# Kernel tuning notes

Measured on AMD Instinct MI355X. Metric: run time of the kernel, lower is better.

Reference implementation:

```python
import jax, jax.numpy as jnp
import numpy as np

DT = 0.1

def setup_inputs() -> dict:
    key = jax.random.key(0)
    ks = jax.random.split(key, 11)
    B, I, H = 65536, 128, 256
    return {
        "x": jax.random.normal(ks[0], (B, I), jnp.float32),
        "prev_input": jax.random.normal(ks[1], (B, I), jnp.float32),
        "hidden": jax.random.normal(ks[2], (B, H), jnp.float32),
        "W_in_w": jax.random.normal(ks[3], (H, I), jnp.float32) * 0.05,
        "W_in_b": jax.random.normal(ks[4], (H,), jnp.float32) * 0.05,
        "W_rec_w": jax.random.normal(ks[5], (H, H), jnp.float32) * 0.05,
        "W_rec_b": jax.random.normal(ks[6], (H,), jnp.float32) * 0.05,
        "attn_w": jax.random.normal(ks[7], (H, H), jnp.float32) * 0.05,
        "attn_b": jax.random.normal(ks[8], (H,), jnp.float32) * 0.05,
        "ev_w": jax.random.normal(ks[9], (1, 2 * I), jnp.float32) * 0.05,
        "ev_b": jax.random.normal(ks[10], (1,), jnp.float32) * 0.05,
        "tau": jnp.ones((H,), jnp.float32),
    }

def reference(x, prev_input, hidden, W_in_w, W_in_b, W_rec_w, W_rec_b,
              attn_w, attn_b, ev_w, ev_b, tau):
    # event detection from concatenated current + previous input
    event_input = jnp.concatenate([x, prev_input], axis=1)  # (B, 2I)
    event_weight = jax.nn.sigmoid(event_input @ ev_w.T + ev_b)  # (B, 1)
    # liquid dynamics
    input_contrib = jnp.tanh(x @ W_in_w.T + W_in_b)  # (B, H)
    attention_weights = jax.nn.sigmoid(hidden @ attn_w.T + attn_b)  # (B, H)
    recurrent_contrib = jnp.tanh((hidden * attention_weights) @ W_rec_w.T + W_rec_b)
    tau_clamped = jnp.clip(tau, 0.1, 10.0)  # (H,)
    dhidden_dt = (-hidden + input_contrib + recurrent_contrib) / tau_clamped
    new_hidden = hidden + DT * dhidden_dt * (1.0 + event_weight)
    return new_hidden, event_weight
```

## Files before the change

kernel.cpp:

```cpp
#include <hip/hip_runtime.h>

#define BI 128
#define BH 256
#define MT 32
#define NT 256

using f32x4  = __attribute__((ext_vector_type(4))) float;
using short8 = __attribute__((ext_vector_type(8))) short;

__device__ __forceinline__ unsigned short f2bf(float f) {
  unsigned u = __float_as_uint(f);
  u = (u + 0x7FFFu + ((u >> 16) & 1u)) >> 16;
  return (unsigned short)u;
}
__device__ __forceinline__ float bf2f(unsigned short h) {
  return __uint_as_float(((unsigned)h) << 16);
}
__device__ __forceinline__ float fast_tanh(float v) {
  return 1.f - 2.f / (1.f + __expf(2.f * v));
}
__device__ __forceinline__ float fast_sigmoid(float v) {
  return 1.f / (1.f + __expf(-v));
}

__global__ void pack_w(const float* __restrict__ W, unsigned short* __restrict__ dst,
                       int K, int total) {
  int t = blockIdx.x * blockDim.x + threadIdx.x;
  if (t >= total) return;
  int lane = t & 63;
  int tile = t >> 6;
  int KT = K >> 5;
  int nf = tile / KT, kt = tile - nf * KT;
  int n  = nf * 16 + (lane & 15);
  int k0 = kt * 32 + (lane >> 4) * 8;
  const float* src = W + (size_t)n * K + k0;
#pragma unroll
  for (int j = 0; j < 8; ++j) dst[(size_t)t * 8 + j] = f2bf(src[j]);
}

__global__ __launch_bounds__(NT, 3) void ha_kernel(
    const float* __restrict__ hidden, const float* __restrict__ attn_b,
    const unsigned short* __restrict__ attn_p,
    unsigned short* __restrict__ ha_out) {
  extern __shared__ char smem[];
  const int tid = threadIdx.x;
  const int lane = tid & 63;
  const int wid = tid >> 6;
  const int r0 = blockIdx.x * MT;
  const int lrow = lane & 15;
  const int lk = lane >> 4;

#pragma unroll
  for (int it = 0; it < 8; ++it) {
    int idx4 = it * NT + tid;
    int row = idx4 >> 6;
    int c = idx4 & 63;
    f32x4 v = *(const f32x4*)(hidden + (size_t)(r0 + row) * BH + c * 4);
    unsigned h01 = (unsigned)f2bf(v[0]) | ((unsigned)f2bf(v[1]) << 16);
    unsigned h23 = (unsigned)f2bf(v[2]) | ((unsigned)f2bf(v[3]) << 16);
    *(unsigned long long*)(smem + row * 512 + ((c * 8) ^ ((row & 7) << 4))) =
        (unsigned long long)h01 | ((unsigned long long)h23 << 32);
  }
  __syncthreads();

  f32x4 acc[2][4] = {};
  {
    const short8* bW = (const short8*)attn_p;
#pragma unroll
    for (int kt = 0; kt < 8; ++kt) {
      short8 ah[2];
#pragma unroll
      for (int mf = 0; mf < 2; ++mf) {
        int row = mf * 16 + lrow;
        ah[mf] = *(const short8*)(smem + row * 512 + ((kt * 64 + lk * 16) ^ ((row & 7) << 4)));
      }
#pragma unroll
      for (int nf = 0; nf < 4; ++nf) {
        short8 b = bW[((wid * 4 + nf) * 8 + kt) * 64 + lane];
#pragma unroll
        for (int mf = 0; mf < 2; ++mf)
          acc[mf][nf] = __builtin_amdgcn_mfma_f32_16x16x32_bf16(ah[mf], b, acc[mf][nf], 0, 0, 0);
      }
    }
  }

#pragma unroll
  for (int nf = 0; nf < 4; ++nf) {
    int col = wid * 64 + nf * 16 + lrow;
    float bb = attn_b[col];
#pragma unroll
    for (int mf = 0; mf < 2; ++mf) {
#pragma unroll
      for (int j = 0; j < 4; ++j) {
        int row = mf * 16 + lk * 4 + j;
        float aw = fast_sigmoid(acc[mf][nf][j] + bb);
        int hoff = row * 512 + ((col * 2) ^ ((row & 7) << 4));
        float h = bf2f(*(const unsigned short*)(smem + hoff));
        *(unsigned short*)(smem + 16384 + hoff) = f2bf(h * aw);
      }
    }
  }
  __syncthreads();

#pragma unroll
  for (int p = 0; p < 4; ++p) {
    int c = p * NT + tid;
    int row = c >> 5;
    int cp = (c & 31) * 16;
    f32x4 v = *(const f32x4*)(smem + 16384 + row * 512 + (cp ^ ((row & 7) << 4)));
    *(f32x4*)((char*)ha_out + (size_t)blockIdx.x * 16384 + (size_t)c * 16) = v;
  }
}

__global__ __launch_bounds__(NT, 3) void liq_kernel(
    const float* __restrict__ x, const float* __restrict__ prev,
    const float* __restrict__ hidden,
    const float* __restrict__ w_in_b, const float* __restrict__ w_rec_b,
    const float* __restrict__ ev_w, const float* __restrict__ ev_b,
    const float* __restrict__ tau,
    const unsigned short* __restrict__ win_p, const unsigned short* __restrict__ wrec_p,
    const unsigned short* __restrict__ ha_in,
    float* __restrict__ out, int Bn) {
  extern __shared__ char smem[];
  const int tid = threadIdx.x;
  const int lane = tid & 63;
  const int wid = tid >> 6;
  const int r0 = blockIdx.x * MT;
  const int lrow = lane & 15;
  const int lk = lane >> 4;

#pragma unroll
  for (int p = 0; p < 4; ++p) {
    int c = p * NT + tid;
    int row = c >> 5;
    int cp = (c & 31) * 16;
    f32x4 v = *(const f32x4*)((const char*)ha_in + (size_t)blockIdx.x * 16384 + (size_t)c * 16);
    *(f32x4*)(smem + row * 512 + (cp ^ ((row & 7) << 4))) = v;
  }

  {
    int r = tid >> 3, p = tid & 7;
    float s = 0.f;
    const float* src = (p < 4) ? (x + (size_t)(r0 + r) * BI + p * 32)
                               : (prev + (size_t)(r0 + r) * BI + (p - 4) * 32);
    const float* wr = ev_w + p * 32;
#pragma unroll
    for (int i = 0; i < 8; ++i) {
      f32x4 a = *(const f32x4*)(src + i * 4);
      f32x4 w = *(const f32x4*)(wr + i * 4);
      s += a[0] * w[0] + a[1] * w[1] + a[2] * w[2] + a[3] * w[3];
    }
    s += __shfl_xor(s, 1);
    s += __shfl_xor(s, 2);
    s += __shfl_xor(s, 4);
    if (p == 0) {
      float ew = fast_sigmoid(s + ev_b[0]);
      *(float*)(smem + 49152 + r * 4) = ew;
      out[(size_t)Bn * BH + r0 + r] = ew;
    }
  }
  __syncthreads();

  {
    f32x4 ic[2][4] = {};
    const short8* bW = (const short8*)win_p;
#pragma unroll
    for (int kt = 0; kt < 4; ++kt) {
      short8 ax[2];
#pragma unroll
      for (int mf = 0; mf < 2; ++mf) {
        const float* xr = x + (size_t)(r0 + mf * 16 + lrow) * BI + kt * 32 + lk * 8;
        f32x4 a0 = *(const f32x4*)xr;
        f32x4 a1 = *(const f32x4*)(xr + 4);
        short8 t;
        t[0] = (short)f2bf(a0[0]); t[1] = (short)f2bf(a0[1]);
        t[2] = (short)f2bf(a0[2]); t[3] = (short)f2bf(a0[3]);
        t[4] = (short)f2bf(a1[0]); t[5] = (short)f2bf(a1[1]);
        t[6] = (short)f2bf(a1[2]); t[7] = (short)f2bf(a1[3]);
        ax[mf] = t;
      }
#pragma unroll
      for (int nf = 0; nf < 4; ++nf) {
        short8 b = bW[((wid * 4 + nf) * 4 + kt) * 64 + lane];
#pragma unroll
        for (int mf = 0; mf < 2; ++mf)
          ic[mf][nf] = __builtin_amdgcn_mfma_f32_16x16x32_bf16(ax[mf], b, ic[mf][nf], 0, 0, 0);
      }
    }
#pragma unroll
    for (int nf = 0; nf < 4; ++nf) {
      int col = wid * 64 + nf * 16 + lrow;
      float bb = w_in_b[col];
#pragma unroll
      for (int mf = 0; mf < 2; ++mf) {
#pragma unroll
        for (int j = 0; j < 4; ++j) {
          int row = mf * 16 + lk * 4 + j;
          *(float*)(smem + 16384 + row * 1024 + ((col * 4) ^ ((row & 7) << 4))) =
              fast_tanh(ic[mf][nf][j] + bb);
        }
      }
    }
  }

  {
    f32x4 rcc[2][4] = {};
    const short8* bW = (const short8*)wrec_p;
#pragma unroll
    for (int kt = 0; kt < 8; ++kt) {
      short8 ah[2];
#pragma unroll
      for (int mf = 0; mf < 2; ++mf) {
        int row = mf * 16 + lrow;
        ah[mf] = *(const short8*)(smem + row * 512 + ((kt * 64 + lk * 16) ^ ((row & 7) << 4)));
      }
#pragma unroll
      for (int nf = 0; nf < 4; ++nf) {
        short8 b = bW[((wid * 4 + nf) * 8 + kt) * 64 + lane];
#pragma unroll
        for (int mf = 0; mf < 2; ++mf)
          rcc[mf][nf] = __builtin_amdgcn_mfma_f32_16x16x32_bf16(ah[mf], b, rcc[mf][nf], 0, 0, 0);
      }
    }
#pragma unroll
    for (int nf = 0; nf < 4; ++nf) {
      int col = wid * 64 + nf * 16 + lrow;
      float brec = w_rec_b[col];
#pragma unroll
      for (int mf = 0; mf < 2; ++mf) {
#pragma unroll
        for (int j = 0; j < 4; ++j) {
          int row = mf * 16 + lk * 4 + j;
          int off = 16384 + row * 1024 + ((col * 4) ^ ((row & 7) << 4));
          float icv = *(const float*)(smem + off);
          *(float*)(smem + off) = icv + fast_tanh(rcc[mf][nf][j] + brec);
        }
      }
    }
  }
  __syncthreads();

  {
    f32x4 t4 = *(const f32x4*)(tau + lane * 4);
    f32x4 dtt;
#pragma unroll
    for (int i = 0; i < 4; ++i) {
      float t = fminf(fmaxf(t4[i], 0.1f), 10.f);
      dtt[i] = 0.1f / t;
    }
#pragma unroll
    for (int it = 0; it < 8; ++it) {
      int row = it * 4 + wid;
      float e1 = 1.f + *(const float*)(smem + 49152 + row * 4);
      f32x4 s4 = *(const f32x4*)(smem + 16384 + row * 1024 + ((lane * 16) ^ ((row & 7) << 4)));
      f32x4 h4 = *(const f32x4*)(hidden + (size_t)(r0 + row) * BH + lane * 4);
      f32x4 o;
#pragma unroll
      for (int i = 0; i < 4; ++i)
        o[i] = h4[i] + dtt[i] * (s4[i] - h4[i]) * e1;
      *(f32x4*)(out + (size_t)(r0 + row) * BH + lane * 4) = o;
    }
  }
}

extern "C" void kernel_launch(void* const* d_in, const int* in_sizes, int n_in,
                              void* d_out, int out_size, void* d_ws, size_t ws_size,
                              hipStream_t stream) {
  const float* x       = (const float*)d_in[0];
  const float* prev    = (const float*)d_in[1];
  const float* hidden  = (const float*)d_in[2];
  const float* W_in_w  = (const float*)d_in[3];
  const float* W_in_b  = (const float*)d_in[4];
  const float* W_rec_w = (const float*)d_in[5];
  const float* W_rec_b = (const float*)d_in[6];
  const float* attn_w  = (const float*)d_in[7];
  const float* attn_b  = (const float*)d_in[8];
  const float* ev_w    = (const float*)d_in[9];
  const float* ev_b    = (const float*)d_in[10];
  const float* tau     = (const float*)d_in[11];
  int Bn = in_sizes[0] / BI;

  unsigned short* ws = (unsigned short*)d_ws;
  unsigned short* win_p  = ws;
  unsigned short* attn_p = ws + 32768;
  unsigned short* wrec_p = ws + 98304;
  unsigned short* ha_ws  = ws + 163840;

  pack_w<<<(4096 + 255) / 256, 256, 0, stream>>>(W_in_w, win_p, BI, 4096);
  pack_w<<<(8192 + 255) / 256, 256, 0, stream>>>(attn_w, attn_p, BH, 8192);
  pack_w<<<(8192 + 255) / 256, 256, 0, stream>>>(W_rec_w, wrec_p, BH, 8192);

  ha_kernel<<<Bn / MT, NT, 32768, stream>>>(hidden, attn_b, attn_p, ha_ws);

  liq_kernel<<<Bn / MT, NT, 49280, stream>>>(
      x, prev, hidden, W_in_b, W_rec_b, ev_w, ev_b, tau,
      win_p, wrec_p, ha_ws, (float*)d_out, Bn);
}
```

Baseline: 120.5 us.

## Split fused liquid kernel into input/event kernel and recurrent update kernel

Splits the single fused kernel into one that computes the event weight and tanh input contribution, writing them to the output buffer, and one that computes the recurrent contribution and final hidden update by reading those back. Each kernel uses less shared memory, and the recurrent tanh is stored as bf16 in LDS, to allow more resident blocks. The cost is an extra full-size fp32 round trip through global memory for the input contribution, plus an extra kernel launch and slightly reduced precision.

```diff
diff --git a/kernel.cpp b/kernel.cpp
--- a/kernel.cpp
+++ b/kernel.cpp
@@ -112,14 +112,11 @@
   }
 }
 
-__global__ __launch_bounds__(NT, 3) void liq_kernel(
+__global__ __launch_bounds__(NT, 3) void icew_kernel(
     const float* __restrict__ x, const float* __restrict__ prev,
-    const float* __restrict__ hidden,
-    const float* __restrict__ w_in_b, const float* __restrict__ w_rec_b,
+    const float* __restrict__ w_in_b,
     const float* __restrict__ ev_w, const float* __restrict__ ev_b,
-    const float* __restrict__ tau,
-    const unsigned short* __restrict__ win_p, const unsigned short* __restrict__ wrec_p,
-    const unsigned short* __restrict__ ha_in,
+    const unsigned short* __restrict__ win_p,
     float* __restrict__ out, int Bn) {
   extern __shared__ char smem[];
   const int tid = threadIdx.x;
@@ -129,15 +126,6 @@
   const int lrow = lane & 15;
   const int lk = lane >> 4;
 
-#pragma unroll
-  for (int p = 0; p < 4; ++p) {
-    int c = p * NT + tid;
-    int row = c >> 5;
-    int cp = (c & 31) * 16;
-    f32x4 v = *(const f32x4*)((const char*)ha_in + (size_t)blockIdx.x * 16384 + (size_t)c * 16);
-    *(f32x4*)(smem + row * 512 + (cp ^ ((row & 7) << 4))) = v;
-  }
-
   {
     int r = tid >> 3, p = tid & 7;
     float s = 0.f;
@@ -153,16 +141,12 @@
     s += __shfl_xor(s, 1);
     s += __shfl_xor(s, 2);
     s += __shfl_xor(s, 4);
-    if (p == 0) {
-      float ew = fast_sigmoid(s + ev_b[0]);
-      *(float*)(smem + 49152 + r * 4) = ew;
-      out[(size_t)Bn * BH + r0 + r] = ew;
-    }
-  }
-  __syncthreads();
-
-  {
-    f32x4 ic[2][4] = {};
+    if (p == 0)
+      out[(size_t)Bn * BH + r0 + r] = fast_sigmoid(s + ev_b[0]);
+  }
+
+  f32x4 ic[2][4] = {};
+  {
     const short8* bW = (const short8*)win_p;
 #pragma unroll
     for (int kt = 0; kt < 4; ++kt) {
@@ -187,24 +171,58 @@
           ic[mf][nf] = __builtin_amdgcn_mfma_f32_16x16x32_bf16(ax[mf], b, ic[mf][nf], 0, 0, 0);
       }
     }
-#pragma unroll
-    for (int nf = 0; nf < 4; ++nf) {
-      int col = wid * 64 + nf * 16 + lrow;
-      float bb = w_in_b[col];
-#pragma unroll
-      for (int mf = 0; mf < 2; ++mf) {
-#pragma unroll
-        for (int j = 0; j < 4; ++j) {
-          int row = mf * 16 + lk * 4 + j;
-          *(float*)(smem + 16384 + row * 1024 + ((col * 4) ^ ((row & 7) << 4))) =
-              fast_tanh(ic[mf][nf][j] + bb);
-        }
-      }
-    }
-  }
-
-  {
-    f32x4 rcc[2][4] = {};
+  }
+
+#pragma unroll
+  for (int nf = 0; nf < 4; ++nf) {
+    int col = wid * 64 + nf * 16 + lrow;
+    float bb = w_in_b[col];
+#pragma unroll
+    for (int mf = 0; mf < 2; ++mf) {
+#pragma unroll
+      for (int j = 0; j < 4; ++j) {
+        int row = mf * 16 + lk * 4 + j;
+        *(float*)(smem + row * 1024 + ((col * 4) ^ ((row & 7) << 4))) =
+            fast_tanh(ic[mf][nf][j] + bb);
+      }
+    }
+  }
+  __syncthreads();
+
+#pragma unroll
+  for (int it = 0; it < 8; ++it) {
+    int row = it * 4 + wid;
+    f32x4 v = *(const f32x4*)(smem + row * 1024 + ((lane * 16) ^ ((row & 7) << 4)));
+    *(f32x4*)(out + (size_t)(r0 + row) * BH + lane * 4) = v;
+  }
+}
+
+__global__ __launch_bounds__(NT, 3) void rec_kernel(
+    const float* __restrict__ hidden, const float* __restrict__ w_rec_b,
+    const float* __restrict__ tau,
+    const unsigned short* __restrict__ wrec_p,
+    const unsigned short* __restrict__ ha_in,
+    float* __restrict__ out, int Bn) {
+  extern __shared__ char smem[];
+  const int tid = threadIdx.x;
+  const int lane = tid & 63;
+  const int wid = tid >> 6;
+  const int r0 = blockIdx.x * MT;
+  const int lrow = lane & 15;
+  const int lk = lane >> 4;
+
+#pragma unroll
+  for (int p = 0; p < 4; ++p) {
+    int c = p * NT + tid;
+    int row = c >> 5;
+    int cp = (c & 31) * 16;
+    f32x4 v = *(const f32x4*)((const char*)ha_in + (size_t)blockIdx.x * 16384 + (size_t)c * 16);
+    *(f32x4*)(smem + row * 512 + (cp ^ ((row & 7) << 4))) = v;
+  }
+  __syncthreads();
+
+  f32x4 rcc[2][4] = {};
+  {
     const short8* bW = (const short8*)wrec_p;
 #pragma unroll
     for (int kt = 0; kt < 8; ++kt) {
@@ -222,19 +240,20 @@
           rcc[mf][nf] = __builtin_amdgcn_mfma_f32_16x16x32_bf16(ah[mf], b, rcc[mf][nf], 0, 0, 0);
       }
     }
-#pragma unroll
-    for (int nf = 0; nf < 4; ++nf) {
-      int col = wid * 64 + nf * 16 + lrow;
-      float brec = w_rec_b[col];
-#pragma unroll
-      for (int mf = 0; mf < 2; ++mf) {
-#pragma unroll
-        for (int j = 0; j < 4; ++j) {
-          int row = mf * 16 + lk * 4 + j;
-          int off = 16384 + row * 1024 + ((col * 4) ^ ((row & 7) << 4));
-          float icv = *(const float*)(smem + off);
-          *(float*)(smem + off) = icv + fast_tanh(rcc[mf][nf][j] + brec);
-        }
+  }
+  __syncthreads();
+
+#pragma unroll
+  for (int nf = 0; nf < 4; ++nf) {
+    int col = wid * 64 + nf * 16 + lrow;
+    float brec = w_rec_b[col];
+#pragma unroll
+    for (int mf = 0; mf < 2; ++mf) {
+#pragma unroll
+      for (int j = 0; j < 4; ++j) {
+        int row = mf * 16 + lk * 4 + j;
+        *(unsigned short*)(smem + row * 512 + ((col * 2) ^ ((row & 7) << 4))) =
+            f2bf(fast_tanh(rcc[mf][nf][j] + brec));
       }
     }
   }
@@ -251,14 +270,19 @@
 #pragma unroll
     for (int it = 0; it < 8; ++it) {
       int row = it * 4 + wid;
-      float e1 = 1.f + *(const float*)(smem + 49152 + row * 4);
-      f32x4 s4 = *(const f32x4*)(smem + 16384 + row * 1024 + ((lane * 16) ^ ((row & 7) << 4)));
+      float e1 = 1.f + out[(size_t)Bn * BH + r0 + row];
+      unsigned long long sv = *(const unsigned long long*)(
+          smem + row * 512 + ((lane * 8) ^ ((row & 7) << 4)));
+      float* orow = out + (size_t)(r0 + row) * BH + lane * 4;
+      f32x4 ic4 = *(const f32x4*)orow;
       f32x4 h4 = *(const f32x4*)(hidden + (size_t)(r0 + row) * BH + lane * 4);
       f32x4 o;
 #pragma unroll
-      for (int i = 0; i < 4; ++i)
-        o[i] = h4[i] + dtt[i] * (s4[i] - h4[i]) * e1;
-      *(f32x4*)(out + (size_t)(r0 + row) * BH + lane * 4) = o;
+      for (int i = 0; i < 4; ++i) {
+        float s = bf2f((unsigned short)(sv >> (16 * i)));
+        o[i] = h4[i] + dtt[i] * (ic4[i] + s - h4[i]) * e1;
+      }
+      *(f32x4*)orow = o;
     }
   }
 }
@@ -292,7 +316,9 @@
 
   ha_kernel<<<Bn / MT, NT, 32768, stream>>>(hidden, attn_b, attn_p, ha_ws);
 
-  liq_kernel<<<Bn / MT, NT, 49280, stream>>>(
-      x, prev, hidden, W_in_b, W_rec_b, ev_w, ev_b, tau,
-      win_p, wrec_p, ha_ws, (float*)d_out, Bn);
-}
+  icew_kernel<<<Bn / MT, NT, 32768, stream>>>(
+      x, prev, W_in_b, ev_w, ev_b, win_p, (float*)d_out, Bn);
+
+  rec_kernel<<<Bn / MT, NT, 16384, stream>>>(
+      hidden, W_rec_b, tau, wrec_p, ha_ws, (float*)d_out, Bn);
+}
```

After: 128.1 us. 1.06x slower.
